# Kernel optimization log

Measured on AMD Instinct MI355X. Metric: run time of the kernel, lower is better.

The kernel has to match this reference:

```python
import jax, jax.numpy as jnp
import numpy as np

D_MODEL = 64  # angle_dist_dim
IN_CH = 256
EPS = 1e-6


def sinusoidal_embedding(e, d_model):
    # e: (N, K) -> (N, K, d_model), interleaved [sin0, cos0, sin1, cos1, ...]
    div_term = jnp.exp(jnp.arange(0, d_model, 2, dtype=jnp.float32) * (-np.log(10000.0) / d_model))
    om = e[..., None] * div_term  # (N, K, d_model//2)
    emb = jnp.stack([jnp.sin(om), jnp.cos(om)], axis=-1)  # (N, K, d/2, 2)
    return emb.reshape(e.shape + (d_model,))


def setup_inputs() -> dict:
    key = jax.random.key(0)
    ks = jax.random.split(key, 5)
    N, K, C = 40000, 16, IN_CH
    triplet_dim = 2 * C + D_MODEL  # 576
    x = jax.random.normal(ks[0], (N, C), dtype=jnp.float32)
    pos = jax.random.normal(ks[1], (N, 3), dtype=jnp.float32) * 10.0
    anchor_indices = jnp.arange(N, dtype=jnp.int32)
    corner_indices = jax.random.randint(ks[2], (N, K, 2), 0, N, dtype=jnp.int32)
    corner_masks = jnp.ones((N, K), dtype=bool)
    Wqkv_w = jax.random.normal(ks[3], (3 * C, triplet_dim), dtype=jnp.float32) / np.sqrt(triplet_dim)
    Wqkv_b = jax.random.normal(ks[4], (3 * C,), dtype=jnp.float32) * 0.01
    return {"x": x, "pos": pos, "anchor_indices": anchor_indices,
            "corner_indices": corner_indices, "corner_masks": corner_masks,
            "Wqkv_w": Wqkv_w, "Wqkv_b": Wqkv_b}


def reference(x, pos, anchor_indices, corner_indices, corner_masks, Wqkv_w, Wqkv_b):
    N, C = x.shape
    padded_x = jnp.concatenate([x, jnp.zeros((1, C), x.dtype)], axis=0)
    padded_pos = jnp.concatenate([pos, jnp.zeros((1, 3), pos.dtype)], axis=0)

    anchor_p = padded_pos[anchor_indices]            # (Na, 3)
    v0 = padded_pos[corner_indices[:, :, 0]] - anchor_p[:, None]  # (Na, K, 3)
    v1 = padded_pos[corner_indices[:, :, 1]] - anchor_p[:, None]
    v0 = jax.lax.stop_gradient(v0).at[:, :, 2].set(0.0)  # zero z (detached geometry)
    v1 = jax.lax.stop_gradient(v1).at[:, :, 2].set(0.0)

    cos_values = jnp.sum(v0 * v1, axis=-1) / (
        jnp.linalg.norm(v0, axis=-1) * jnp.linalg.norm(v1, axis=-1) + EPS)
    # z-component of cross product (x,y only since z was zeroed)
    sin_z = v0[..., 0] * v1[..., 1] - v0[..., 1] * v1[..., 0]
    reorder = sin_z < 0  # (Na, K)

    ci = jnp.where(reorder[..., None], corner_indices[:, :, ::-1], corner_indices)

    nv0 = jax.lax.stop_gradient(padded_pos[ci[:, :, 0]] - anchor_p[:, None]).at[:, :, 2].set(0.0)
    nv1 = jax.lax.stop_gradient(padded_pos[ci[:, :, 1]] - anchor_p[:, None]).at[:, :, 2].set(0.0)
    new_sin_z = nv0[..., 0] * nv1[..., 1] - nv0[..., 1] * nv1[..., 0]
    # corner_masks is all-True so boolean selection == full flatten (static shape)
    triplet_false_masks = ((new_sin_z < -1e-6) & corner_masks).reshape(-1)

    angle_features = jax.lax.stop_gradient(sinusoidal_embedding(cos_values, D_MODEL))
    triplet_feats = jnp.concatenate(
        [padded_x[ci[:, :, 0]], padded_x[ci[:, :, 1]], angle_features], axis=-1)  # (Na, K, 576)

    qkv = triplet_feats @ Wqkv_w.T + Wqkv_b            # (Na, K, 3C)
    qkv = qkv.reshape(qkv.shape[0], qkv.shape[1], 3, C)
    q, k, v = qkv[:, :, 0], qkv[:, :, 1], qkv[:, :, 2]

    scores = jnp.einsum('nqc,nkc->nqk', q, k) / np.sqrt(C)
    attn = jax.nn.softmax(scores, axis=-1)
    attn_feats = jnp.einsum('nqk,nkc->nqc', attn, v)   # (Na, K, C)

    mask_f = corner_masks.astype(attn_feats.dtype)
    denom = jnp.sum(mask_f, axis=1, keepdims=True)     # (Na, 1)
    mean_feats = jnp.sum(attn_feats * mask_f[..., None], axis=1) / denom  # (Na, C)

    x_messages = jnp.zeros_like(x).at[anchor_indices].set(mean_feats)
    out = jnp.concatenate([x, x_messages], axis=1)     # (N, 2C), triplet_mlp_method='concat'
    return out, triplet_false_masks
```

## Files before the change

### kernel.cpp

```cpp
#include <hip/hip_runtime.h>

typedef unsigned short u16;
typedef __attribute__((ext_vector_type(8))) short short8v;
typedef __attribute__((ext_vector_type(4))) float float4v;

__device__ __forceinline__ float bf2f(u16 u) {
  union { unsigned int i; float f; } v; v.i = ((unsigned int)u) << 16; return v.f;
}
__device__ __forceinline__ u16 f2bf(float f) {
  union { unsigned int i; float f; } v; v.f = f;
  unsigned int r = v.i + 0x7fffu + ((v.i >> 16) & 1u);
  return (u16)(r >> 16);
}
__device__ __forceinline__ float4v mfma_bf16(short8v a, short8v b, float4v c) {
  return __builtin_amdgcn_mfma_f32_16x16x32_bf16(a, b, c, 0, 0, 0);
}

__global__ __launch_bounds__(256) void prep_kernel(const float* __restrict__ W,
                                                   u16* __restrict__ Bt,
                                                   u16* __restrict__ W2t) {
  int j = blockIdx.x;
  int c = threadIdx.x;
  const float* wr = W + (size_t)j * 576;
  Bt[(size_t)j * 256 + c]         = f2bf(wr[c]);
  Bt[(size_t)(768 + j) * 256 + c] = f2bf(wr[256 + c]);
  if (c < 64) W2t[(size_t)j * 64 + c] = f2bf(wr[512 + c]);
}

__global__ __launch_bounds__(256) void gemm_kernel(const float* __restrict__ A,
                                                   const u16* __restrict__ Bt,
                                                   u16* __restrict__ Y, int M) {
  __shared__ __align__(16) u16 As[128][72];
  __shared__ __align__(16) u16 Bs[128][72];
  int tid = threadIdx.x;
  int row0 = blockIdx.x * 128, col0 = blockIdx.y * 128;
  int w = tid >> 6, l = tid & 63;
  int wr = w >> 1, wc = w & 1;
  int lr = l & 15, lq = l >> 4;

  float4v acc[4][4];
#pragma unroll
  for (int mi = 0; mi < 4; mi++)
#pragma unroll
    for (int ni = 0; ni < 4; ni++) acc[mi][ni] = (float4v)0.f;

  for (int k0 = 0; k0 < 256; k0 += 64) {
#pragma unroll
    for (int i = 0; i < 4; i++) {
      int chunk = tid + i * 256;
      int r = chunk >> 3;
      int kc = (chunk & 7) * 8;
      int gr = row0 + r;
      short8v av = (short8v)0;
      if (gr < M) {
        float4 f0 = *(const float4*)(A + (size_t)gr * 256 + k0 + kc);
        float4 f1 = *(const float4*)(A + (size_t)gr * 256 + k0 + kc + 4);
        av[0] = (short)f2bf(f0.x); av[1] = (short)f2bf(f0.y);
        av[2] = (short)f2bf(f0.z); av[3] = (short)f2bf(f0.w);
        av[4] = (short)f2bf(f1.x); av[5] = (short)f2bf(f1.y);
        av[6] = (short)f2bf(f1.z); av[7] = (short)f2bf(f1.w);
      }
      *(short8v*)&As[r][kc] = av;
      short8v bv = *(const short8v*)(Bt + (size_t)(col0 + r) * 256 + k0 + kc);
      *(short8v*)&Bs[r][kc] = bv;
    }
    __syncthreads();
#pragma unroll
    for (int s = 0; s < 2; s++) {
      int kb = s * 32 + lq * 8;
      short8v af[4], bf[4];
#pragma unroll
      for (int mi = 0; mi < 4; mi++)
        af[mi] = *(const short8v*)&As[wr * 64 + mi * 16 + lr][kb];
#pragma unroll
      for (int ni = 0; ni < 4; ni++)
        bf[ni] = *(const short8v*)&Bs[wc * 64 + ni * 16 + lr][kb];
#pragma unroll
      for (int mi = 0; mi < 4; mi++)
#pragma unroll
        for (int ni = 0; ni < 4; ni++)
          acc[mi][ni] = mfma_bf16(af[mi], bf[ni], acc[mi][ni]);
    }
    __syncthreads();
  }
#pragma unroll
  for (int mi = 0; mi < 4; mi++)
#pragma unroll
    for (int ni = 0; ni < 4; ni++) {
      int rbase = row0 + wr * 64 + mi * 16 + lq * 4;
      int c = col0 + wc * 64 + ni * 16 + lr;
#pragma unroll
      for (int j = 0; j < 4; j++) {
        int r = rbase + j;
        if (r < M) Y[(size_t)r * 1536 + c] = f2bf(acc[mi][ni][j]);
      }
    }
}

__global__ __launch_bounds__(64, 4) void triplet_kernel(
    const float* __restrict__ x, const float* __restrict__ pos,
    const int* __restrict__ anchor, const int* __restrict__ corner,
    const float* __restrict__ bias, const u16* __restrict__ Y,
    const u16* __restrict__ W2t, float* __restrict__ out, int N) {
  __shared__ __align__(16) u16 s_t[16][72];

  int n = blockIdx.x;
  if (n >= N) return;
  int l = threadIdx.x;
  int lr = l & 15, lq = l >> 4, kg = lq * 8;
  int a = anchor[n];

  int2 ci = ((const int2*)corner)[n * 16 + lr];
  float ax = pos[(size_t)a * 3], ay = pos[(size_t)a * 3 + 1];
  float v0x = pos[(size_t)ci.x * 3]     - ax;
  float v0y = pos[(size_t)ci.x * 3 + 1] - ay;
  float v1x = pos[(size_t)ci.y * 3]     - ax;
  float v1y = pos[(size_t)ci.y * 3 + 1] - ay;
  float dotv = v0x * v1x + v0y * v1y;
  float n0 = sqrtf(v0x * v0x + v0y * v0y);
  float n1 = sqrtf(v1x * v1x + v1y * v1y);
  float cosv = dotv / (n0 * n1 + 1e-6f);
  bool sw = (v0x * v1y - v0y * v1x) < 0.f;
  int i0 = sw ? ci.y : ci.x;
  int i1 = sw ? ci.x : ci.y;

  if (l < 16) out[(size_t)N * 512 + (size_t)n * 16 + l] = 0.0f;
  {
    float4 v = ((const float4*)(x + (size_t)n * 256))[l];
    ((float4*)(out + (size_t)n * 512))[l] = v;
  }

  short8v a0, a1;
#pragma unroll
  for (int j = 0; j < 8; j++) {
    int k = kg + j;
    float om0 = cosv * __expf(-0.28782313662425572f * (float)(k >> 1));
    a0[j] = (short)f2bf((k & 1) ? __cosf(om0) : __sinf(om0));
    int k2 = 32 + kg + j;
    float om1 = cosv * __expf(-0.28782313662425572f * (float)(k2 >> 1));
    a1[j] = (short)f2bf((k2 & 1) ? __cosf(om1) : __sinf(om1));
  }

  const u16* y0 = Y + (size_t)i0 * 1536;
  const u16* y1 = Y + (size_t)i1 * 1536 + 768;

  float4v sacc = (float4v)0.f;
  for (int cs = 0; cs < 8; cs++) {
    __syncthreads();
#pragma unroll
    for (int gi = 0; gi < 4; gi++) {
      int g = (gi < 2) ? (cs * 2 + gi) : (16 + cs * 2 + (gi - 2));
      const u16* wrow = W2t + (size_t)(g * 16 + lr) * 64;
      short8v wa = *(const short8v*)(wrow + kg);
      short8v wb = *(const short8v*)(wrow + 32 + kg);
      float4v d = mfma_bf16(wb, a1, (float4v)0.f);
      d = mfma_bf16(wa, a0, d);
      uint2 pv;
      pv.x = (unsigned)f2bf(d[0]) | ((unsigned)f2bf(d[1]) << 16);
      pv.y = (unsigned)f2bf(d[2]) | ((unsigned)f2bf(d[3]) << 16);
      *(uint2*)&s_t[lr][gi * 16 + lq * 4] = pv;
    }
    __syncthreads();
    int cq = cs * 32 + kg;
    int ck = 256 + cs * 32 + kg;
    short8v tq = *(const short8v*)&s_t[lr][kg];
    short8v tk = *(const short8v*)&s_t[lr][32 + kg];
    short8v gq0 = *(const short8v*)(y0 + cq);
    short8v gq1 = *(const short8v*)(y1 + cq);
    short8v gk0 = *(const short8v*)(y0 + ck);
    short8v gk1 = *(const short8v*)(y1 + ck);
    union { float4 v[2]; float f[8]; } bq, bk;
    bq.v[0] = *(const float4*)(bias + cq); bq.v[1] = *(const float4*)(bias + cq + 4);
    bk.v[0] = *(const float4*)(bias + ck); bk.v[1] = *(const float4*)(bias + ck + 4);
    short8v qf, kf;
#pragma unroll
    for (int j = 0; j < 8; j++) {
      float qv = bf2f((u16)tq[j]) + bq.f[j] + bf2f((u16)gq0[j]) + bf2f((u16)gq1[j]);
      qf[j] = (short)f2bf(qv);
      float kv = bf2f((u16)tk[j]) + bk.f[j] + bf2f((u16)gk0[j]) + bf2f((u16)gk1[j]);
      kf[j] = (short)f2bf(kv);
    }
    sacc = mfma_bf16(qf, kf, sacc);
  }

  float wsum = 0.f;
#pragma unroll
  for (int j = 0; j < 4; j++) {
    float s = sacc[j] * 0.0625f;
    float m = s;
    m = fmaxf(m, __shfl_xor(m, 1));
    m = fmaxf(m, __shfl_xor(m, 2));
    m = fmaxf(m, __shfl_xor(m, 4));
    m = fmaxf(m, __shfl_xor(m, 8));
    float e = __expf(s - m);
    float sm = e;
    sm += __shfl_xor(sm, 1);
    sm += __shfl_xor(sm, 2);
    sm += __shfl_xor(sm, 4);
    sm += __shfl_xor(sm, 8);
    wsum += e / sm;
  }
  wsum += __shfl_xor(wsum, 16);
  wsum += __shfl_xor(wsum, 32);
  wsum *= 0.0625f;

  float* op = out + (size_t)a * 512 + 256;
  for (int cs = 0; cs < 8; cs++) {
    __syncthreads();
#pragma unroll
    for (int gi = 0; gi < 2; gi++) {
      int g = 32 + cs * 2 + gi;
      const u16* wrow = W2t + (size_t)(g * 16 + lr) * 64;
      short8v wa = *(const short8v*)(wrow + kg);
      short8v wb = *(const short8v*)(wrow + 32 + kg);
      float4v d = mfma_bf16(wb, a1, (float4v)0.f);
      d = mfma_bf16(wa, a0, d);
      uint2 pv;
      pv.x = (unsigned)f2bf(d[0]) | ((unsigned)f2bf(d[1]) << 16);
      pv.y = (unsigned)f2bf(d[2]) | ((unsigned)f2bf(d[3]) << 16);
      *(uint2*)&s_t[lr][gi * 16 + lq * 4] = pv;
    }
    __syncthreads();
    int cv = 512 + cs * 32 + kg;
    short8v tv = *(const short8v*)&s_t[lr][kg];
    short8v gv0 = *(const short8v*)(y0 + cv);
    short8v gv1 = *(const short8v*)(y1 + cv);
    union { float4 v[2]; float f[8]; } bv;
    bv.v[0] = *(const float4*)(bias + cv); bv.v[1] = *(const float4*)(bias + cv + 4);
    float o[8];
#pragma unroll
    for (int j = 0; j < 8; j++) {
      float vv = bf2f((u16)tv[j]) + bv.f[j] + bf2f((u16)gv0[j]) + bf2f((u16)gv1[j]);
      float p = wsum * vv;
      p += __shfl_xor(p, 1);
      p += __shfl_xor(p, 2);
      p += __shfl_xor(p, 4);
      p += __shfl_xor(p, 8);
      o[j] = p;
    }
    if (lr == 0) {
      float4 o0, o1;
      o0.x = o[0]; o0.y = o[1]; o0.z = o[2]; o0.w = o[3];
      o1.x = o[4]; o1.y = o[5]; o1.z = o[6]; o1.w = o[7];
      *(float4*)(op + cs * 32 + kg) = o0;
      *(float4*)(op + cs * 32 + kg + 4) = o1;
    }
  }
}

extern "C" void kernel_launch(void* const* d_in, const int* in_sizes, int n_in,
                              void* d_out, int out_size, void* d_ws, size_t ws_size,
                              hipStream_t stream) {
  const float* x    = (const float*)d_in[0];
  const float* pos  = (const float*)d_in[1];
  const int* anchor = (const int*)d_in[2];
  const int* corner = (const int*)d_in[3];
  const float* W    = (const float*)d_in[5];
  const float* bias = (const float*)d_in[6];
  float* out = (float*)d_out;
  int N = in_sizes[2];

  char* wsb = (char*)d_ws;
  u16* Bt  = (u16*)wsb;
  u16* W2t = (u16*)(wsb + 786432);
  u16* Y   = (u16*)(wsb + 786432 + 98304);

  prep_kernel<<<768, 256, 0, stream>>>(W, Bt, W2t);
  gemm_kernel<<<dim3((N + 127) / 128, 12), 256, 0, stream>>>(x, Bt, Y, N);
  triplet_kernel<<<N, 64, 0, stream>>>(x, pos, anchor, corner, bias, Y, W2t, out, N);
}
```

Baseline: 904.6 us.

## Consume angle-GEMM MFMA outputs in registers, drop LDS transpose, prefetch gathers

The angle-embedding projection results are now used directly in the MFMA accumulator layout. The Q/K channel permutation is chosen so the accumulator layout matches the A/B operand layout of the score MFMA, which removes the shared-memory staging buffer and both barriers per chunk. Gathered Y rows are software-prefetched one chunk ahead and the loops are fully unrolled. It also drops the intermediate bf16 rounding of the angle term, at the cost of higher register pressure under the 4-wave occupancy bound.

```diff
diff --git a/kernel.cpp b/kernel.cpp
--- a/kernel.cpp
+++ b/kernel.cpp
@@ -97,17 +97,33 @@
     }
 }
 
+__device__ __forceinline__ float4v tgrp(const u16* __restrict__ W2t, int g,
+                                        int lr, int kg, short8v a0, short8v a1) {
+  const u16* wrow = W2t + (size_t)(g * 16 + lr) * 64;
+  short8v wa = *(const short8v*)(wrow + kg);
+  short8v wb = *(const short8v*)(wrow + 32 + kg);
+  float4v d = mfma_bf16(wa, a0, (float4v)0.f);
+  return mfma_bf16(wb, a1, d);
+}
+
+__device__ __forceinline__ void acc4(float4v d, float4 b, uint2 g0, uint2 g1,
+                                     float* o) {
+  o[0] = d[0] + b.x + bf2f((u16)(g0.x & 0xffffu)) + bf2f((u16)(g1.x & 0xffffu));
+  o[1] = d[1] + b.y + bf2f((u16)(g0.x >> 16))     + bf2f((u16)(g1.x >> 16));
+  o[2] = d[2] + b.z + bf2f((u16)(g0.y & 0xffffu)) + bf2f((u16)(g1.y & 0xffffu));
+  o[3] = d[3] + b.w + bf2f((u16)(g0.y >> 16))     + bf2f((u16)(g1.y >> 16));
+}
+
 __global__ __launch_bounds__(64, 4) void triplet_kernel(
     const float* __restrict__ x, const float* __restrict__ pos,
     const int* __restrict__ anchor, const int* __restrict__ corner,
     const float* __restrict__ bias, const u16* __restrict__ Y,
     const u16* __restrict__ W2t, float* __restrict__ out, int N) {
-  __shared__ __align__(16) u16 s_t[16][72];
-
   int n = blockIdx.x;
   if (n >= N) return;
   int l = threadIdx.x;
   int lr = l & 15, lq = l >> 4, kg = lq * 8;
+  int cho = lq * 4;
   int a = anchor[n];
 
   int2 ci = ((const int2*)corner)[n * 16 + lr];
@@ -145,40 +161,50 @@
   const u16* y1 = Y + (size_t)i1 * 1536 + 768;
 
   float4v sacc = (float4v)0.f;
+  uint2 q0a = *(const uint2*)(y0 + cho);
+  uint2 q1a = *(const uint2*)(y1 + cho);
+  uint2 q0b = *(const uint2*)(y0 + 16 + cho);
+  uint2 q1b = *(const uint2*)(y1 + 16 + cho);
+  uint2 k0a = *(const uint2*)(y0 + 256 + cho);
+  uint2 k1a = *(const uint2*)(y1 + 256 + cho);
+  uint2 k0b = *(const uint2*)(y0 + 256 + 16 + cho);
+  uint2 k1b = *(const uint2*)(y1 + 256 + 16 + cho);
+#pragma unroll
   for (int cs = 0; cs < 8; cs++) {
-    __syncthreads();
-#pragma unroll
-    for (int gi = 0; gi < 4; gi++) {
-      int g = (gi < 2) ? (cs * 2 + gi) : (16 + cs * 2 + (gi - 2));
-      const u16* wrow = W2t + (size_t)(g * 16 + lr) * 64;
-      short8v wa = *(const short8v*)(wrow + kg);
-      short8v wb = *(const short8v*)(wrow + 32 + kg);
-      float4v d = mfma_bf16(wb, a1, (float4v)0.f);
-      d = mfma_bf16(wa, a0, d);
-      uint2 pv;
-      pv.x = (unsigned)f2bf(d[0]) | ((unsigned)f2bf(d[1]) << 16);
-      pv.y = (unsigned)f2bf(d[2]) | ((unsigned)f2bf(d[3]) << 16);
-      *(uint2*)&s_t[lr][gi * 16 + lq * 4] = pv;
-    }
-    __syncthreads();
-    int cq = cs * 32 + kg;
-    int ck = 256 + cs * 32 + kg;
-    short8v tq = *(const short8v*)&s_t[lr][kg];
-    short8v tk = *(const short8v*)&s_t[lr][32 + kg];
-    short8v gq0 = *(const short8v*)(y0 + cq);
-    short8v gq1 = *(const short8v*)(y1 + cq);
-    short8v gk0 = *(const short8v*)(y0 + ck);
-    short8v gk1 = *(const short8v*)(y1 + ck);
-    union { float4 v[2]; float f[8]; } bq, bk;
-    bq.v[0] = *(const float4*)(bias + cq); bq.v[1] = *(const float4*)(bias + cq + 4);
-    bk.v[0] = *(const float4*)(bias + ck); bk.v[1] = *(const float4*)(bias + ck + 4);
+    uint2 cq0a = q0a, cq1a = q1a, cq0b = q0b, cq1b = q1b;
+    uint2 ck0a = k0a, ck1a = k1a, ck0b = k0b, ck1b = k1b;
+    if (cs < 7) {
+      int c = (cs + 1) * 32 + cho;
+      q0a = *(const uint2*)(y0 + c);
+      q1a = *(const uint2*)(y1 + c);
+      q0b = *(const uint2*)(y0 + c + 16);
+      q1b = *(const uint2*)(y1 + c + 16);
+      k0a = *(const uint2*)(y0 + 256 + c);
+      k1a = *(const uint2*)(y1 + 256 + c);
+      k0b = *(const uint2*)(y0 + 256 + c + 16);
+      k1b = *(const uint2*)(y1 + 256 + c + 16);
+    }
+    float4v dQa = tgrp(W2t, 2 * cs,      lr, kg, a0, a1);
+    float4v dQb = tgrp(W2t, 2 * cs + 1,  lr, kg, a0, a1);
+    float4v dKa = tgrp(W2t, 16 + 2 * cs, lr, kg, a0, a1);
+    float4v dKb = tgrp(W2t, 17 + 2 * cs, lr, kg, a0, a1);
+    int cb = cs * 32 + cho;
+    float4 bqa = *(const float4*)(bias + cb);
+    float4 bqb = *(const float4*)(bias + cb + 16);
+    float4 bka = *(const float4*)(bias + 256 + cb);
+    float4 bkb = *(const float4*)(bias + 256 + cb + 16);
+    float oqa[4], oqb[4], oka[4], okb[4];
+    acc4(dQa, bqa, cq0a, cq1a, oqa);
+    acc4(dQb, bqb, cq0b, cq1b, oqb);
+    acc4(dKa, bka, ck0a, ck1a, oka);
+    acc4(dKb, bkb, ck0b, ck1b, okb);
     short8v qf, kf;
 #pragma unroll
-    for (int j = 0; j < 8; j++) {
-      float qv = bf2f((u16)tq[j]) + bq.f[j] + bf2f((u16)gq0[j]) + bf2f((u16)gq1[j]);
-      qf[j] = (short)f2bf(qv);
-      float kv = bf2f((u16)tk[j]) + bk.f[j] + bf2f((u16)gk0[j]) + bf2f((u16)gk1[j]);
-      kf[j] = (short)f2bf(kv);
+    for (int j = 0; j < 4; j++) {
+      qf[j]     = (short)f2bf(oqa[j]);
+      qf[4 + j] = (short)f2bf(oqb[j]);
+      kf[j]     = (short)f2bf(oka[j]);
+      kf[4 + j] = (short)f2bf(okb[j]);
     }
     sacc = mfma_bf16(qf, kf, sacc);
   }
@@ -205,45 +231,32 @@
   wsum *= 0.0625f;
 
   float* op = out + (size_t)a * 512 + 256;
-  for (int cs = 0; cs < 8; cs++) {
-    __syncthreads();
-#pragma unroll
-    for (int gi = 0; gi < 2; gi++) {
-      int g = 32 + cs * 2 + gi;
-      const u16* wrow = W2t + (size_t)(g * 16 + lr) * 64;
-      short8v wa = *(const short8v*)(wrow + kg);
-      short8v wb = *(const short8v*)(wrow + 32 + kg);
-      float4v d = mfma_bf16(wb, a1, (float4v)0.f);
-      d = mfma_bf16(wa, a0, d);
-      uint2 pv;
-      pv.x = (unsigned)f2bf(d[0]) | ((unsigned)f2bf(d[1]) << 16);
-      pv.y = (unsigned)f2bf(d[2]) | ((unsigned)f2bf(d[3]) << 16);
-      *(uint2*)&s_t[lr][gi * 16 + lq * 4] = pv;
-    }
-    __syncthreads();
-    int cv = 512 + cs * 32 + kg;
-    short8v tv = *(const short8v*)&s_t[lr][kg];
-    short8v gv0 = *(const short8v*)(y0 + cv);
-    short8v gv1 = *(const short8v*)(y1 + cv);
-    union { float4 v[2]; float f[8]; } bv;
-    bv.v[0] = *(const float4*)(bias + cv); bv.v[1] = *(const float4*)(bias + cv + 4);
-    float o[8];
-#pragma unroll
-    for (int j = 0; j < 8; j++) {
-      float vv = bf2f((u16)tv[j]) + bv.f[j] + bf2f((u16)gv0[j]) + bf2f((u16)gv1[j]);
-      float p = wsum * vv;
+  uint2 v0 = *(const uint2*)(y0 + 512 + cho);
+  uint2 v1 = *(const uint2*)(y1 + 512 + cho);
+#pragma unroll
+  for (int g = 0; g < 16; g++) {
+    uint2 cv0 = v0, cv1 = v1;
+    if (g < 15) {
+      int c = 512 + (g + 1) * 16 + cho;
+      v0 = *(const uint2*)(y0 + c);
+      v1 = *(const uint2*)(y1 + c);
+    }
+    float4v dv = tgrp(W2t, 32 + g, lr, kg, a0, a1);
+    float4 bv = *(const float4*)(bias + 512 + g * 16 + cho);
+    float o[4];
+    acc4(dv, bv, cv0, cv1, o);
+#pragma unroll
+    for (int r = 0; r < 4; r++) {
+      float p = wsum * o[r];
       p += __shfl_xor(p, 1);
       p += __shfl_xor(p, 2);
       p += __shfl_xor(p, 4);
       p += __shfl_xor(p, 8);
-      o[j] = p;
+      o[r] = p;
     }
     if (lr == 0) {
-      float4 o0, o1;
-      o0.x = o[0]; o0.y = o[1]; o0.z = o[2]; o0.w = o[3];
-      o1.x = o[4]; o1.y = o[5]; o1.z = o[6]; o1.w = o[7];
-      *(float4*)(op + cs * 32 + kg) = o0;
-      *(float4*)(op + cs * 32 + kg + 4) = o1;
+      float4 ov; ov.x = o[0]; ov.y = o[1]; ov.z = o[2]; ov.w = o[3];
+      *(float4*)(op + g * 16 + cho) = ov;
     }
   }
 }
```

Result: slower. 1.108 ms (+22.4%).
